# Kernel optimization log

Measured on AMD Instinct MI355X. Metric: run time of the kernel, lower is better.

## Reference

```python
import jax, jax.numpy as jnp
import numpy as np

B, N, K = 256, 4096, 64


def setup_inputs() -> dict:
    key = jax.random.key(0)
    k0, k1, k2, k3, k4 = jax.random.split(key, 5)
    targets = jax.random.uniform(k0, (B, N), dtype=jnp.float32)
    rho = jnp.array([0.25], dtype=jnp.float32)
    qs = jax.random.uniform(k1, (B, N), minval=0.05, maxval=0.95, dtype=jnp.float32)
    means = 0.1 * jax.random.normal(k2, (B, N), dtype=jnp.float32)
    C = 0.1 * jax.random.normal(k3, (K, N), dtype=jnp.float32)
    psi_diag = jax.random.uniform(k4, (N,), minval=0.1, maxval=1.1, dtype=jnp.float32)
    return {"targets": targets, "rho": rho, "qs": qs, "means": means, "C": C, "psi_diag": psi_diag}


def _zif_loglikelihood(targets, rho_s, qs, means, C, psi_diag, gmask):
    # gmask: bool [B,N], detached (constant) as in the torch original
    m = gmask.astype(targets.dtype)            # gaussian mask as float
    umask = 1.0 - m                            # uniform mask
    # uniform part: sum over uniform entries of log(1-q) - log(rho)
    uniform_lp = ((jnp.log1p(-qs) - jnp.log(rho_s)) * umask).sum(axis=1)  # [B]
    # sample_transform: elementwise log transform on masked entries
    t_safe = jnp.where(gmask, targets, 1.0)
    y = jnp.log(t_safe)                        # transformed targets
    logdet_elem = -jnp.log(t_safe)             # log|d y / d t| per element
    # masked low-rank Gaussian log_prob via Woodbury (cov = C^T C + diag(psi) on masked subset)
    d = (y - means) * m                        # residual, zero outside mask  [B,N]
    w = m / psi_diag                           # masked inverse diag          [B,N]
    A = jnp.einsum('bn,kn,ln->bkl', w, C, C) + jnp.eye(K, dtype=targets.dtype)  # I + W^T D^-1 W  [B,K,K]
    u = jnp.einsum('bn,kn->bk', w * d, C)      # W^T D^-1 d                   [B,K]
    L = jnp.linalg.cholesky(A)
    logdetA = 2.0 * jnp.sum(jnp.log(jnp.diagonal(L, axis1=-2, axis2=-1)), axis=-1)  # [B]
    Ainv_u = jnp.linalg.solve(A, u[..., None])[..., 0]                              # [B,K]
    quad = jnp.sum(w * d * d, axis=1) - jnp.sum(u * Ainv_u, axis=1)                 # Mahalanobis [B]
    n_b = m.sum(axis=1)                                                             # ragged sizes
    logdet_cov = jnp.sum(m * jnp.log(psi_diag), axis=1) + logdetA
    gauss_lp = -0.5 * (n_b * jnp.log(jnp.asarray(2.0 * jnp.pi, targets.dtype)) + logdet_cov + quad)
    extra = jnp.sum(m * logdet_elem, axis=1) + jnp.sum(m * jnp.log(qs), axis=1)
    return uniform_lp + gauss_lp + extra       # [B] loglikelihood per sample


def reference(targets, rho, qs, means, C, psi_diag):
    rho_s = rho[0]
    gmask = targets >= rho_s                   # detached boolean mask
    return _zif_loglikelihood(targets, rho_s, qs, means, C, psi_diag, gmask)
```

## Files before the change

### kernel.cpp

```cpp
#include <hip/hip_runtime.h>
#include <math.h>

#define NNV 4096
#define KKV 64
#define BBV 256
#define CHN 256
#define NCH (NNV / CHN)

typedef unsigned short u16;
typedef unsigned int u32;
typedef u32  u32x4  __attribute__((ext_vector_type(4)));
typedef short bf16x8 __attribute__((ext_vector_type(8)));
typedef float f32x4  __attribute__((ext_vector_type(4)));
typedef float f32x16 __attribute__((ext_vector_type(16)));

__device__ inline u16 f2bf(float x) {
    u32 u = __float_as_uint(x);
    u = u + 0x7FFFu + ((u >> 16) & 1u);
    return (u16)(u >> 16);
}

__device__ inline float rlane(float v, int l) {
    return __uint_as_float(__builtin_amdgcn_readlane(__float_as_uint(v), l));
}

__global__ __launch_bounds__(256) void prep(
    const float* __restrict__ targets, const float* __restrict__ rho,
    const float* __restrict__ qs, const float* __restrict__ means,
    const float* __restrict__ C, const float* __restrict__ psi,
    u16* __restrict__ Csbf, u16* __restrict__ dsbf,
    u32* __restrict__ mask2, float* __restrict__ scal) {
    const int blk = blockIdx.x;
    const int t = threadIdx.x;

    if (blk >= BBV) {
        const int k = blk - BBV;
        const float* Crow = C + (size_t)k * NNV;
        u16* Orow = Csbf + (size_t)k * NNV;
        const int base = t * 16;
#pragma unroll
        for (int j = 0; j < 16; j += 4) {
            float4 cv = *(const float4*)(Crow + base + j);
            float4 pv = *(const float4*)(psi + base + j);
            u32 w0 = (u32)f2bf(cv.x * rsqrtf(pv.x)) | ((u32)f2bf(cv.y * rsqrtf(pv.y)) << 16);
            u32 w1 = (u32)f2bf(cv.z * rsqrtf(pv.z)) | ((u32)f2bf(cv.w * rsqrtf(pv.w)) << 16);
            *(uint2*)(Orow + base + j) = make_uint2(w0, w1);
        }
        return;
    }

    __shared__ float sred[4][5];
    const int b = blk;
    const int lane = t & 63, wid = t >> 6;
    const float rho_s = rho[0];
    const float lrho = __logf(rho_s);
    const int base = t * 16;
    const float* tg = targets + (size_t)b * NNV + base;
    const float* qb = qs + (size_t)b * NNV + base;
    const float* mb = means + (size_t)b * NNV + base;
    const float* pb = psi + base;

    float tvv[16], qv[16], muv[16], pv[16];
#pragma unroll
    for (int j = 0; j < 16; j += 4) {
        *(float4*)(tvv + j) = *(const float4*)(tg + j);
        *(float4*)(qv + j)  = *(const float4*)(qb + j);
        *(float4*)(muv + j) = *(const float4*)(mb + j);
        *(float4*)(pv + j)  = *(const float4*)(pb + j);
    }

    float s_uni = 0.f, s_wdd = 0.f, s_nb = 0.f, s_mlp = 0.f, s_extra = 0.f;
    u16 dsv[16]; bool mk[16];
#pragma unroll
    for (int j = 0; j < 16; ++j) {
        bool m = tvv[j] >= rho_s;
        float ds = 0.f;
        if (m) {
            float y = __logf(tvv[j]);
            float d = y - muv[j];
            ds = d * rsqrtf(pv[j]);
            s_wdd += ds * ds;
            s_nb += 1.f;
            s_mlp += __logf(pv[j]);
            s_extra += __logf(qv[j]) - y;
        } else {
            s_uni += __logf(1.f - qv[j]) - lrho;
        }
        dsv[j] = f2bf(ds);
        mk[j] = m;
    }
    u32 mw[8], dp[8];
#pragma unroll
    for (int i = 0; i < 8; ++i) {
        mw[i] = (mk[2*i] ? 0xFFFFu : 0u) | (mk[2*i+1] ? 0xFFFF0000u : 0u);
        dp[i] = (u32)dsv[2*i] | ((u32)dsv[2*i+1] << 16);
    }
    *(u32x4*)(dsbf + (size_t)b * NNV + base)     = ((u32x4*)dp)[0];
    *(u32x4*)(dsbf + (size_t)b * NNV + base + 8) = ((u32x4*)dp)[1];
    *(u32x4*)(mask2 + (size_t)b * (NNV/2) + t*8)     = ((u32x4*)mw)[0];
    *(u32x4*)(mask2 + (size_t)b * (NNV/2) + t*8 + 4) = ((u32x4*)mw)[1];

#pragma unroll
    for (int off = 32; off > 0; off >>= 1) {
        s_uni  += __shfl_down(s_uni, off);
        s_wdd  += __shfl_down(s_wdd, off);
        s_nb   += __shfl_down(s_nb, off);
        s_mlp  += __shfl_down(s_mlp, off);
        s_extra+= __shfl_down(s_extra, off);
    }
    if (lane == 0) {
        sred[wid][0] = s_uni; sred[wid][1] = s_wdd; sred[wid][2] = s_nb;
        sred[wid][3] = s_mlp; sred[wid][4] = s_extra;
    }
    __syncthreads();
    if (t == 0) {
        float a0=0,a1=0,a2=0,a3=0,a4=0;
#pragma unroll
        for (int w4 = 0; w4 < 4; ++w4) {
            a0 += sred[w4][0]; a1 += sred[w4][1]; a2 += sred[w4][2];
            a3 += sred[w4][3]; a4 += sred[w4][4];
        }
        scal[b*5+0]=a0; scal[b*5+1]=a1; scal[b*5+2]=a2; scal[b*5+3]=a3; scal[b*5+4]=a4;
    }
}

__global__ __launch_bounds__(512) void gram(
    const u16* __restrict__ Csbf, const u16* __restrict__ dsbf,
    const u32* __restrict__ mask2g, float* __restrict__ Abuf, float* __restrict__ Uf) {
    __shared__ __align__(16) u16 gbuf[3][KKV * CHN];
    __shared__ __align__(16) u16 dsrow[3][512];
    __shared__ __align__(16) u32 m2[NNV / 2];

    const int b = blockIdx.x;
    const int t = threadIdx.x;
    const int lane = t & 63;
    const int w = t >> 6;
    const int half = w & 1;
    const int tilid = w >> 1;
    const int l31 = lane & 31;
    const int hsel = lane >> 5;

    {
        u32x4 v = *(const u32x4*)(mask2g + (size_t)b * (NNV/2) + t*4);
        *(u32x4*)(m2 + t*4) = v;
    }

    f32x16 acc;
#pragma unroll
    for (int i = 0; i < 16; ++i) acc[i] = 0.f;
    f32x4 ua, ubv;
#pragma unroll
    for (int i = 0; i < 4; ++i) { ua[i] = 0.f; ubv[i] = 0.f; }

#define STAGE(cc, pp) do {                                                          \
    _Pragma("unroll")                                                               \
    for (int i_ = 0; i_ < 4; ++i_) {                                                \
        int beta0 = w*256 + i_*64;                                                  \
        int beta = beta0 + lane;                                                    \
        int r_ = beta >> 5, blkP = beta & 31;                                       \
        int blkS = blkP ^ (r_ & 15);         \
        const u16* src = Csbf + (size_t)r_ * NNV + (cc)*CHN + blkS*8;               \
        __builtin_amdgcn_global_load_lds(                                           \
            (const __attribute__((address_space(1))) void*)src,                     \
            (__attribute__((address_space(3))) void*)(&gbuf[pp][beta0*8]),          \
            16, 0, 0);                                                              \
    }                                                                               \
    {                                                                               \
        const u16* srcd = dsbf + (size_t)b * NNV + (cc)*CHN + (lane & 31)*8;        \
        __builtin_amdgcn_global_load_lds(                                           \
            (const __attribute__((address_space(1))) void*)srcd,                    \
            (__attribute__((address_space(3))) void*)(&dsrow[pp][0]),               \
            16, 0, 0);                                                              \
    }                                                                               \
} while (0)

    STAGE(0, 0);
    STAGE(1, 1);
    asm volatile("s_waitcnt vmcnt(5) lgkmcnt(0)" ::: "memory");
    __builtin_amdgcn_s_barrier();

#pragma unroll
    for (int c = 0; c < NCH; ++c) {
        const int p = c % 3;
        if (c + 2 < NCH) STAGE(c + 2, (c + 2) % 3);
        const char* gb = (const char*)gbuf[p];
        if (w < 6) {
            const int rbA = (tilid == 0) ? 0 : 32;
            const int rbB = (tilid == 2) ? 32 : 0;
            const int rA = rbA + l31, rB = rbB + l31;
            const int swA = (rA & 15) << 4, swB = (rB & 15) << 4;
            const char* mbase = (const char*)m2 + c*512 + hsel*16;
#pragma unroll
            for (int s8 = 0; s8 < 8; ++s8) {
                const int s = half*8 + s8;
                const int colbyte = s*32 + hsel*16;
                u32x4 fB = *(const u32x4*)(gb + rB*512 + (colbyte ^ swB));
                u32x4 fA;
                if (tilid == 1) fA = *(const u32x4*)(gb + rA*512 + (colbyte ^ swA));
                else            fA = fB;
                u32x4 mkv = *(const u32x4*)(mbase + s*32);
                fA = fA & mkv;
                acc = __builtin_amdgcn_mfma_f32_32x32x16_bf16(
                        __builtin_bit_cast(bf16x8, fA),
                        __builtin_bit_cast(bf16x8, fB), acc, 0, 0, 0);
            }
        } else {
            const int cb0 = (w == 6) ? 0 : 32;
            const int l15 = lane & 15;
            const int g4 = lane >> 4;
            const int r0 = cb0 + l15, r1 = r0 + 16;
            const int sw0 = (r0 & 15) << 4, sw1 = (r1 & 15) << 4;
            const char* dr = (const char*)dsrow[p];
#pragma unroll
            for (int su = 0; su < 8; ++su) {
                const int colbyte = su*64 + g4*16;
                u32x4 dv = *(const u32x4*)(dr + colbyte);
                if (l15 != 0) dv = dv ^ dv;
                u32x4 f0 = *(const u32x4*)(gb + r0*512 + (colbyte ^ sw0));
                u32x4 f1 = *(const u32x4*)(gb + r1*512 + (colbyte ^ sw1));
                ua  = __builtin_amdgcn_mfma_f32_16x16x32_bf16(
                        __builtin_bit_cast(bf16x8, dv), __builtin_bit_cast(bf16x8, f0), ua, 0,0,0);
                ubv = __builtin_amdgcn_mfma_f32_16x16x32_bf16(
                        __builtin_bit_cast(bf16x8, dv), __builtin_bit_cast(bf16x8, f1), ubv, 0,0,0);
            }
        }
        if (c + 2 < NCH) asm volatile("s_waitcnt vmcnt(5) lgkmcnt(0)" ::: "memory");
        else             asm volatile("s_waitcnt vmcnt(0) lgkmcnt(0)" ::: "memory");
        __builtin_amdgcn_s_barrier();
    }

    float* red = (float*)&gbuf[0][0];
    if (w < 6 && half == 0) {
#pragma unroll
        for (int g = 0; g < 16; ++g) {
            int row = (g & 3) + 8*(g >> 2) + 4*hsel;
            red[tilid*1024 + row*32 + l31] = acc[g];
        }
    }
    if (w >= 6 && lane < 16) {
        const int cb0 = (w == 6) ? 0 : 32;
        Uf[b*KKV + cb0 + lane]      = ua[0];
        Uf[b*KKV + cb0 + 16 + lane] = ubv[0];
    }
    __syncthreads();
    if (w < 6 && half == 1) {
#pragma unroll
        for (int g = 0; g < 16; ++g) {
            int row = (g & 3) + 8*(g >> 2) + 4*hsel;
            float v = red[tilid*1024 + row*32 + l31] + acc[g];
            int gr = (tilid == 0) ? row : 32 + row;
            int gc = (tilid == 2) ? 32 + l31 : l31;
            Abuf[(size_t)b*4096 + gr*64 + gc] = v;
        }
    }
#undef STAGE
}

__global__ __launch_bounds__(64, 1) void chol64(
    const float* __restrict__ Abuf, const float* __restrict__ Uf,
    const float* __restrict__ scal, float* __restrict__ out) {
    const int b = blockIdx.x;
    const int lane = threadIdx.x;
    const float* Arow = Abuf + (size_t)b * 4096 + lane * 64;

    float arow[64];
#pragma unroll
    for (int j4 = 0; j4 < 16; ++j4)
        *(float4*)(arow + j4 * 4) = *(const float4*)(Arow + j4 * 4);
    float ubr = Uf[b * 64 + lane];

    float Lrow[64];
    float dval = 1.f, invd = 0.f;
#pragma unroll
    for (int j = 0; j < 64; ++j) {
        float s0 = 0.f, s1 = 0.f, s2 = 0.f, s3 = 0.f;
#pragma unroll
        for (int k = 0; k < (j & ~3); k += 4) {
            s0 += Lrow[k]     * rlane(Lrow[k],     j);
            s1 += Lrow[k + 1] * rlane(Lrow[k + 1], j);
            s2 += Lrow[k + 2] * rlane(Lrow[k + 2], j);
            s3 += Lrow[k + 3] * rlane(Lrow[k + 3], j);
        }
#pragma unroll
        for (int k = (j & ~3); k < j; ++k)
            s0 += Lrow[k] * rlane(Lrow[k], j);
        float a = arow[j] + ((lane == j) ? 1.0f : 0.0f) - ((s0 + s1) + (s2 + s3));
        float dv = rlane(a, j);
        float invs = rsqrtf(dv);
        if (lane == j) { dval = dv; invd = invs; }
        Lrow[j] = (lane > j) ? a * invs : 0.f;
    }

    float z2 = 0.f;
#pragma unroll
    for (int j = 0; j < 64; ++j) {
        float zj = rlane(ubr, j) * rlane(invd, j);
        z2 += zj * zj;
        ubr -= Lrow[j] * zj;
    }

    float ld = __logf(dval);
#pragma unroll
    for (int off = 32; off > 0; off >>= 1) ld += __shfl_xor(ld, off);

    if (lane == 0) {
        float uni = scal[b*5+0], wdd = scal[b*5+1], nb = scal[b*5+2],
              mlp = scal[b*5+3], extra = scal[b*5+4];
        const float LOG2PI = 1.8378770664093453f;
        out[b] = uni + extra - 0.5f * (nb * LOG2PI + mlp + ld + (wdd - z2));
    }
}

extern "C" void kernel_launch(void* const* d_in, const int* in_sizes, int n_in,
                              void* d_out, int out_size, void* d_ws, size_t ws_size,
                              hipStream_t stream) {
    const float* targets = (const float*)d_in[0];
    const float* rho     = (const float*)d_in[1];
    const float* qs      = (const float*)d_in[2];
    const float* means   = (const float*)d_in[3];
    const float* C       = (const float*)d_in[4];
    const float* psi     = (const float*)d_in[5];
    float* out = (float*)d_out;

    char* ws = (char*)d_ws;
    u16* Csbf  = (u16*)(ws);
    u16* dsbf  = (u16*)(ws + 0x80000);
    u32* mask2 = (u32*)(ws + 0x280000);
    float* Abuf = (float*)(ws + 0x480000);
    float* Uf   = (float*)(ws + 0x880000);
    float* scal = (float*)(ws + 0x890000);

    prep<<<BBV + KKV, 256, 0, stream>>>(targets, rho, qs, means, C, psi,
                                        Csbf, dsbf, mask2, scal);
    gram<<<BBV, 512, 0, stream>>>(Csbf, dsbf, mask2, Abuf, Uf);
    chol64<<<BBV, 64, 0, stream>>>(Abuf, Uf, scal, out);
}
```

Measured before the change: 47.89 us.

## Process two batch rows per gram block with N split in halves

Each gram block now handles a pair of batch rows over half of the N dimension. Every staged C chunk is reused for two masked Gram products and two projections, which halves C traffic per sample. The two half-sums are written as partials and added in the Cholesky kernel. The cost is more accumulator registers, a larger partial-output buffer, extra reads in chol64, and a launch_bounds of 2 blocks per CU that may cause register spilling.

```diff
diff --git a/kernel.cpp b/kernel.cpp
--- a/kernel.cpp
+++ b/kernel.cpp
@@ -124,14 +124,19 @@
     }
 }
 
-__global__ __launch_bounds__(512) void gram(
+__global__ __launch_bounds__(512, 2) void gram(
     const u16* __restrict__ Csbf, const u16* __restrict__ dsbf,
-    const u32* __restrict__ mask2g, float* __restrict__ Abuf, float* __restrict__ Uf) {
+    const u32* __restrict__ mask2g, float* __restrict__ Apart, float* __restrict__ Upart) {
     __shared__ __align__(16) u16 gbuf[3][KKV * CHN];
-    __shared__ __align__(16) u16 dsrow[3][512];
-    __shared__ __align__(16) u32 m2[NNV / 2];
-
-    const int b = blockIdx.x;
+    __shared__ __align__(16) u16 dsrow[2][3][512];
+    __shared__ __align__(16) u32 m2[2][NNV / 2];
+
+    const int bid = blockIdx.x;
+    const int nhalf = bid & 1;
+    const int pair = bid >> 1;
+    const int b0 = pair * 2, b1 = b0 + 1;
+    const int c0 = nhalf * (NCH / 2);
+
     const int t = threadIdx.x;
     const int lane = t & 63;
     const int w = t >> 6;
@@ -141,16 +146,18 @@
     const int hsel = lane >> 5;
 
     {
-        u32x4 v = *(const u32x4*)(mask2g + (size_t)b * (NNV/2) + t*4);
-        *(u32x4*)(m2 + t*4) = v;
-    }
-
-    f32x16 acc;
-#pragma unroll
-    for (int i = 0; i < 16; ++i) acc[i] = 0.f;
-    f32x4 ua, ubv;
-#pragma unroll
-    for (int i = 0; i < 4; ++i) { ua[i] = 0.f; ubv[i] = 0.f; }
+        u32x4 v0 = *(const u32x4*)(mask2g + (size_t)b0 * (NNV/2) + t*4);
+        *(u32x4*)(&m2[0][t*4]) = v0;
+        u32x4 v1 = *(const u32x4*)(mask2g + (size_t)b1 * (NNV/2) + t*4);
+        *(u32x4*)(&m2[1][t*4]) = v1;
+    }
+
+    f32x16 acc0, acc1;
+#pragma unroll
+    for (int i = 0; i < 16; ++i) { acc0[i] = 0.f; acc1[i] = 0.f; }
+    f32x4 ua0, ub0, ua1, ub1;
+#pragma unroll
+    for (int i = 0; i < 4; ++i) { ua0[i] = 0.f; ub0[i] = 0.f; ua1[i] = 0.f; ub1[i] = 0.f; }
 
 #define STAGE(cc, pp) do {                                                          \
     _Pragma("unroll")                                                               \
@@ -166,43 +173,55 @@
             16, 0, 0);                                                              \
     }                                                                               \
     {                                                                               \
-        const u16* srcd = dsbf + (size_t)b * NNV + (cc)*CHN + (lane & 31)*8;        \
+        const u16* s0_ = dsbf + (size_t)b0 * NNV + (cc)*CHN + (lane & 31)*8;        \
         __builtin_amdgcn_global_load_lds(                                           \
-            (const __attribute__((address_space(1))) void*)srcd,                    \
-            (__attribute__((address_space(3))) void*)(&dsrow[pp][0]),               \
+            (const __attribute__((address_space(1))) void*)s0_,                     \
+            (__attribute__((address_space(3))) void*)(&dsrow[0][pp][0]),            \
+            16, 0, 0);                                                              \
+        const u16* s1_ = dsbf + (size_t)b1 * NNV + (cc)*CHN + (lane & 31)*8;        \
+        __builtin_amdgcn_global_load_lds(                                           \
+            (const __attribute__((address_space(1))) void*)s1_,                     \
+            (__attribute__((address_space(3))) void*)(&dsrow[1][pp][0]),            \
             16, 0, 0);                                                              \
     }                                                                               \
 } while (0)
 
-    STAGE(0, 0);
-    STAGE(1, 1);
-    asm volatile("s_waitcnt vmcnt(5) lgkmcnt(0)" ::: "memory");
+    STAGE(c0 + 0, 0);
+    STAGE(c0 + 1, 1);
+    asm volatile("s_waitcnt vmcnt(6) lgkmcnt(0)" ::: "memory");
     __builtin_amdgcn_s_barrier();
 
 #pragma unroll
-    for (int c = 0; c < NCH; ++c) {
-        const int p = c % 3;
-        if (c + 2 < NCH) STAGE(c + 2, (c + 2) % 3);
+    for (int cl = 0; cl < NCH / 2; ++cl) {
+        const int c = c0 + cl;
+        const int p = cl % 3;
+        if (cl + 2 < NCH / 2) STAGE(c0 + cl + 2, (cl + 2) % 3);
         const char* gb = (const char*)gbuf[p];
         if (w < 6) {
             const int rbA = (tilid == 0) ? 0 : 32;
             const int rbB = (tilid == 2) ? 32 : 0;
             const int rA = rbA + l31, rB = rbB + l31;
             const int swA = (rA & 15) << 4, swB = (rB & 15) << 4;
-            const char* mbase = (const char*)m2 + c*512 + hsel*16;
+            const char* mb0 = (const char*)&m2[0][0] + c*512 + hsel*16;
+            const char* mb1 = (const char*)&m2[1][0] + c*512 + hsel*16;
 #pragma unroll
             for (int s8 = 0; s8 < 8; ++s8) {
                 const int s = half*8 + s8;
                 const int colbyte = s*32 + hsel*16;
                 u32x4 fB = *(const u32x4*)(gb + rB*512 + (colbyte ^ swB));
-                u32x4 fA;
-                if (tilid == 1) fA = *(const u32x4*)(gb + rA*512 + (colbyte ^ swA));
-                else            fA = fB;
-                u32x4 mkv = *(const u32x4*)(mbase + s*32);
-                fA = fA & mkv;
-                acc = __builtin_amdgcn_mfma_f32_32x32x16_bf16(
-                        __builtin_bit_cast(bf16x8, fA),
-                        __builtin_bit_cast(bf16x8, fB), acc, 0, 0, 0);
+                u32x4 fAr;
+                if (tilid == 1) fAr = *(const u32x4*)(gb + rA*512 + (colbyte ^ swA));
+                else            fAr = fB;
+                u32x4 mk0 = *(const u32x4*)(mb0 + s*32);
+                u32x4 mk1 = *(const u32x4*)(mb1 + s*32);
+                u32x4 fA0 = fAr & mk0;
+                u32x4 fA1 = fAr & mk1;
+                acc0 = __builtin_amdgcn_mfma_f32_32x32x16_bf16(
+                        __builtin_bit_cast(bf16x8, fA0),
+                        __builtin_bit_cast(bf16x8, fB), acc0, 0, 0, 0);
+                acc1 = __builtin_amdgcn_mfma_f32_32x32x16_bf16(
+                        __builtin_bit_cast(bf16x8, fA1),
+                        __builtin_bit_cast(bf16x8, fB), acc1, 0, 0, 0);
             }
         } else {
             const int cb0 = (w == 6) ? 0 : 32;
@@ -210,64 +229,85 @@
             const int g4 = lane >> 4;
             const int r0 = cb0 + l15, r1 = r0 + 16;
             const int sw0 = (r0 & 15) << 4, sw1 = (r1 & 15) << 4;
-            const char* dr = (const char*)dsrow[p];
+            const char* dr0 = (const char*)&dsrow[0][p][0];
+            const char* dr1 = (const char*)&dsrow[1][p][0];
 #pragma unroll
             for (int su = 0; su < 8; ++su) {
                 const int colbyte = su*64 + g4*16;
-                u32x4 dv = *(const u32x4*)(dr + colbyte);
-                if (l15 != 0) dv = dv ^ dv;
+                u32x4 dv0 = *(const u32x4*)(dr0 + colbyte);
+                u32x4 dv1 = *(const u32x4*)(dr1 + colbyte);
+                if (l15 != 0) { dv0 = dv0 ^ dv0; dv1 = dv1 ^ dv1; }
                 u32x4 f0 = *(const u32x4*)(gb + r0*512 + (colbyte ^ sw0));
                 u32x4 f1 = *(const u32x4*)(gb + r1*512 + (colbyte ^ sw1));
-                ua  = __builtin_amdgcn_mfma_f32_16x16x32_bf16(
-                        __builtin_bit_cast(bf16x8, dv), __builtin_bit_cast(bf16x8, f0), ua, 0,0,0);
-                ubv = __builtin_amdgcn_mfma_f32_16x16x32_bf16(
-                        __builtin_bit_cast(bf16x8, dv), __builtin_bit_cast(bf16x8, f1), ubv, 0,0,0);
+                ua0 = __builtin_amdgcn_mfma_f32_16x16x32_bf16(
+                        __builtin_bit_cast(bf16x8, dv0), __builtin_bit_cast(bf16x8, f0), ua0, 0,0,0);
+                ub0 = __builtin_amdgcn_mfma_f32_16x16x32_bf16(
+                        __builtin_bit_cast(bf16x8, dv0), __builtin_bit_cast(bf16x8, f1), ub0, 0,0,0);
+                ua1 = __builtin_amdgcn_mfma_f32_16x16x32_bf16(
+                        __builtin_bit_cast(bf16x8, dv1), __builtin_bit_cast(bf16x8, f0), ua1, 0,0,0);
+                ub1 = __builtin_amdgcn_mfma_f32_16x16x32_bf16(
+                        __builtin_bit_cast(bf16x8, dv1), __builtin_bit_cast(bf16x8, f1), ub1, 0,0,0);
             }
         }
-        if (c + 2 < NCH) asm volatile("s_waitcnt vmcnt(5) lgkmcnt(0)" ::: "memory");
-        else             asm volatile("s_waitcnt vmcnt(0) lgkmcnt(0)" ::: "memory");
+        if (cl + 2 < NCH / 2) asm volatile("s_waitcnt vmcnt(6) lgkmcnt(0)" ::: "memory");
+        else                  asm volatile("s_waitcnt vmcnt(0) lgkmcnt(0)" ::: "memory");
         __builtin_amdgcn_s_barrier();
     }
 
-    float* red = (float*)&gbuf[0][0];
+    float* red0 = (float*)&gbuf[0][0];
+    float* red1 = (float*)&gbuf[1][0];
     if (w < 6 && half == 0) {
 #pragma unroll
         for (int g = 0; g < 16; ++g) {
             int row = (g & 3) + 8*(g >> 2) + 4*hsel;
-            red[tilid*1024 + row*32 + l31] = acc[g];
+            red0[tilid*1024 + row*32 + l31] = acc0[g];
+            red1[tilid*1024 + row*32 + l31] = acc1[g];
         }
     }
     if (w >= 6 && lane < 16) {
         const int cb0 = (w == 6) ? 0 : 32;
-        Uf[b*KKV + cb0 + lane]      = ua[0];
-        Uf[b*KKV + cb0 + 16 + lane] = ubv[0];
+        float* U0 = Upart + ((size_t)nhalf * BBV + b0) * KKV;
+        float* U1 = Upart + ((size_t)nhalf * BBV + b1) * KKV;
+        U0[cb0 + lane]      = ua0[0];
+        U0[cb0 + 16 + lane] = ub0[0];
+        U1[cb0 + lane]      = ua1[0];
+        U1[cb0 + 16 + lane] = ub1[0];
     }
     __syncthreads();
     if (w < 6 && half == 1) {
+        float* A0 = Apart + ((size_t)nhalf * BBV + b0) * 4096;
+        float* A1 = Apart + ((size_t)nhalf * BBV + b1) * 4096;
 #pragma unroll
         for (int g = 0; g < 16; ++g) {
             int row = (g & 3) + 8*(g >> 2) + 4*hsel;
-            float v = red[tilid*1024 + row*32 + l31] + acc[g];
             int gr = (tilid == 0) ? row : 32 + row;
             int gc = (tilid == 2) ? 32 + l31 : l31;
-            Abuf[(size_t)b*4096 + gr*64 + gc] = v;
+            A0[gr*64 + gc] = red0[tilid*1024 + row*32 + l31] + acc0[g];
+            A1[gr*64 + gc] = red1[tilid*1024 + row*32 + l31] + acc1[g];
         }
     }
 #undef STAGE
 }
 
 __global__ __launch_bounds__(64, 1) void chol64(
-    const float* __restrict__ Abuf, const float* __restrict__ Uf,
+    const float* __restrict__ Apart, const float* __restrict__ Upart,
     const float* __restrict__ scal, float* __restrict__ out) {
     const int b = blockIdx.x;
     const int lane = threadIdx.x;
-    const float* Arow = Abuf + (size_t)b * 4096 + lane * 64;
+    const float* Ar0 = Apart + (size_t)b * 4096 + lane * 64;
+    const float* Ar1 = Apart + ((size_t)BBV + b) * 4096 + lane * 64;
 
     float arow[64];
 #pragma unroll
-    for (int j4 = 0; j4 < 16; ++j4)
-        *(float4*)(arow + j4 * 4) = *(const float4*)(Arow + j4 * 4);
-    float ubr = Uf[b * 64 + lane];
+    for (int j4 = 0; j4 < 16; ++j4) {
+        float4 v0 = *(const float4*)(Ar0 + j4 * 4);
+        float4 v1 = *(const float4*)(Ar1 + j4 * 4);
+        arow[j4*4+0] = v0.x + v1.x;
+        arow[j4*4+1] = v0.y + v1.y;
+        arow[j4*4+2] = v0.z + v1.z;
+        arow[j4*4+3] = v0.w + v1.w;
+    }
+    float ubr = Upart[b * 64 + lane] + Upart[(BBV + b) * 64 + lane];
 
     float Lrow[64];
     float dval = 1.f, invd = 0.f;
@@ -323,15 +363,15 @@
     float* out = (float*)d_out;
 
     char* ws = (char*)d_ws;
-    u16* Csbf  = (u16*)(ws);
-    u16* dsbf  = (u16*)(ws + 0x80000);
-    u32* mask2 = (u32*)(ws + 0x280000);
-    float* Abuf = (float*)(ws + 0x480000);
-    float* Uf   = (float*)(ws + 0x880000);
-    float* scal = (float*)(ws + 0x890000);
+    u16* Csbf   = (u16*)(ws);
+    u16* dsbf   = (u16*)(ws + 0x80000);
+    u32* mask2  = (u32*)(ws + 0x280000);
+    float* Apart = (float*)(ws + 0x480000);
+    float* Upart = (float*)(ws + 0xC80000);
+    float* scal  = (float*)(ws + 0xCC0000);
 
     prep<<<BBV + KKV, 256, 0, stream>>>(targets, rho, qs, means, C, psi,
                                         Csbf, dsbf, mask2, scal);
-    gram<<<BBV, 512, 0, stream>>>(Csbf, dsbf, mask2, Abuf, Uf);
-    chol64<<<BBV, 64, 0, stream>>>(Abuf, Uf, scal, out);
-}
+    gram<<<BBV, 512, 0, stream>>>(Csbf, dsbf, mask2, Apart, Upart);
+    chol64<<<BBV, 64, 0, stream>>>(Apart, Upart, scal, out);
+}
```

After: 45.28 us. 1.06x faster.
